# Kernel optimization log

Measured on AMD Instinct MI355X. Metric: run time of the kernel, lower is better.

Reference implementation:

```python
import jax, jax.numpy as jnp
import numpy as np

EPS = 1e-5

def _ln(x, w):
    # LayerNorm over last dim, elementwise affine weight, no bias
    m = jnp.mean(x, axis=-1, keepdims=True)
    v = jnp.mean((x - m) ** 2, axis=-1, keepdims=True)
    return (x - m) * jax.lax.rsqrt(v + EPS) * w

def setup_inputs() -> dict:
    key = jax.random.key(0)
    ks = jax.random.split(key, 16)
    B, NP, NC, E, C = 1, 512, 128, 256, 128
    s = 0.02
    return {
        "z": jax.random.normal(ks[0], (B, NP, NC, E), jnp.float32),
        "protein_pair": jax.random.normal(ks[1], (B, NP, NP, E), jnp.float32),
        "compound_pair": jax.random.normal(ks[2], (B, NC, NC, E), jnp.float32),
        "z_mask": jnp.ones((B, NP, NC, 1), jnp.float32),
        "ln_w": jnp.ones((E,), jnp.float32),
        "lnc_w": jnp.ones((C,), jnp.float32),
        "gw1": jax.random.normal(ks[3], (E, C), jnp.float32) * s,
        "gw2": jax.random.normal(ks[4], (E, C), jnp.float32) * s,
        "w1": jax.random.normal(ks[5], (E, C), jnp.float32) * s,
        "b1": jax.random.normal(ks[6], (C,), jnp.float32) * s,
        "w2": jax.random.normal(ks[7], (E, C), jnp.float32) * s,
        "b2": jax.random.normal(ks[8], (C,), jnp.float32) * s,
        "we": jax.random.normal(ks[9], (E, E), jnp.float32) * s,
        "be": jax.random.normal(ks[10], (E,), jnp.float32) * s,
        "ws": jax.random.normal(ks[11], (C, E), jnp.float32) * s,
        "bs": jax.random.normal(ks[12], (E,), jnp.float32) * s,
    }

def reference(z, protein_pair, compound_pair, z_mask,
              ln_w, lnc_w, gw1, gw2, w1, b1, w2, b2, we, be, ws, bs):
    z = _ln(z, ln_w)                       # [b,Np,Nc,E]
    pp = _ln(protein_pair, ln_w)           # [b,Np,Np,E]
    cp = _ln(compound_pair, ln_w)          # [b,Nc,Nc,E]
    ab1 = jax.nn.sigmoid(z @ gw1) * (z @ w1 + b1) * z_mask   # [b,Np,Nc,c]
    ab2 = jax.nn.sigmoid(z @ gw2) * (z @ w2 + b2) * z_mask   # [b,Np,Nc,c]
    pp = jax.nn.sigmoid(pp @ gw2) * (pp @ w2 + b2)           # [b,Np,Np,c]
    cp = jax.nn.sigmoid(cp @ gw1) * (cp @ w1 + b1)           # [b,Nc,Nc,c]
    g = jax.nn.sigmoid(z @ we + be)                          # [b,Np,Nc,E]
    block1 = jnp.einsum('bikc,bkjc->bijc', pp, ab1)          # [b,Np,Nc,c]
    block2 = jnp.einsum('bikc,bjkc->bijc', ab2, cp)          # [b,Np,Nc,c]
    out = g * (_ln(block1 + block2, lnc_w) @ ws + bs) * z_mask
    return out
```

## Files before the change

### kernel.cpp

```cpp
#include <hip/hip_runtime.h>
#include <hip/hip_bf16.h>

#define NPv 512
#define NCv 128
#define Ev  256
#define Cv  128

typedef __attribute__((ext_vector_type(4))) float f32x4;
typedef __attribute__((ext_vector_type(8))) short s16x8;

__device__ __forceinline__ unsigned short f2bf(float f) {
    union { float f; unsigned u; } v; v.f = f;
    unsigned r = v.u + 0x7fffu + ((v.u >> 16) & 1u);
    return (unsigned short)(r >> 16);
}
__device__ __forceinline__ float bf2f(unsigned short h) {
    union { unsigned u; float f; } v; v.u = ((unsigned)h) << 16;
    return v.f;
}
__device__ __forceinline__ float sigmoidf_(float x) {
    return 1.0f / (1.0f + __expf(-x));
}
__device__ __forceinline__ f32x4 mfma16(s16x8 a, s16x8 b, f32x4 c) {
    return __builtin_amdgcn_mfma_f32_16x16x32_bf16(a, b, c, 0, 0, 0);
}

__global__ void prep_weights(const float* __restrict__ gw1, const float* __restrict__ w1,
                             const float* __restrict__ gw2, const float* __restrict__ w2,
                             const float* __restrict__ we,  const float* __restrict__ wsm,
                             unsigned short* __restrict__ out)
{
    int o = blockIdx.x * 256 + threadIdx.x;
    const float* src; int N, KC; size_t base; int lo;
    if (o < 131072)      { int mi = o >> 15; lo = o & 32767; N = 128; KC = 8;
                           base = (size_t)mi * 32768;
                           src = (mi == 0) ? gw1 : (mi == 1) ? w1 : (mi == 2) ? gw2 : w2; }
    else if (o < 196608) { lo = o - 131072; N = 256; KC = 8; base = 131072; src = we; }
    else                 { lo = o - 196608; N = 256; KC = 4; base = 196608; src = wsm; }
    int e    = lo & 7;
    int lane = (lo >> 3) & 63;
    int blk  = lo >> 9;
    int kc   = blk % KC, nb = blk / KC;
    int n = nb * 16 + (lane & 15);
    int k = kc * 32 + ((lane >> 4) << 3) + e;
    out[base + lo] = f2bf(src[(size_t)k * N + n]);
}

template<int HAS2, int HASG, int HASMASK>
__global__ __launch_bounds__(256, HAS2 ? 3 : 4)
void ln_gate_kernel(const float* __restrict__ X, int M,
                    const float* __restrict__ lnw,
                    const unsigned short* __restrict__ Bu1, const unsigned short* __restrict__ Bv1,
                    const float* __restrict__ bias1, unsigned short* __restrict__ out1,
                    const unsigned short* __restrict__ Bu2, const unsigned short* __restrict__ Bv2,
                    const float* __restrict__ bias2, unsigned short* __restrict__ out2,
                    const unsigned short* __restrict__ Bwe, const float* __restrict__ be,
                    unsigned short* __restrict__ gout,
                    const float* __restrict__ mask)
{
    __shared__ __align__(16) char smem[HAS2 ? (33792 + 18432) : 33792];
    unsigned short (*A_s)[264] = reinterpret_cast<unsigned short(*)[264]>(smem);
    unsigned short (*T_s)[72]  = reinterpret_cast<unsigned short(*)[72]>(
                                     smem + (HAS2 ? 33792 : 0));
    const int t = threadIdx.x;
    const int lane = t & 63, w = t >> 6;
    const int l15 = lane & 15, lg = lane >> 4;
    const int m0 = blockIdx.x * 64;
    const int wy = w >> 1, wx = w & 1;

    float4 lwv[4];
    #pragma unroll
    for (int q = 0; q < 4; q++)
        lwv[q] = *reinterpret_cast<const float4*>(lnw + l15 * 16 + q * 4);
    #pragma unroll
    for (int i = 0; i < 4; i++) {
        const int r = w * 16 + i * 4 + lg;
        const float* xp = X + (size_t)(m0 + r) * Ev + l15 * 16;
        float4 xv[4];
        #pragma unroll
        for (int q = 0; q < 4; q++) xv[q] = *reinterpret_cast<const float4*>(xp + q * 4);
        float s = 0.f, s2 = 0.f;
        #pragma unroll
        for (int q = 0; q < 4; q++) {
            s  += xv[q].x + xv[q].y + xv[q].z + xv[q].w;
            s2 += xv[q].x * xv[q].x + xv[q].y * xv[q].y
                + xv[q].z * xv[q].z + xv[q].w * xv[q].w;
        }
        #pragma unroll
        for (int o = 1; o < 16; o <<= 1) { s += __shfl_xor(s, o); s2 += __shfl_xor(s2, o); }
        float mean = s * (1.0f / Ev);
        float var  = s2 * (1.0f / Ev) - mean * mean;
        float rstd = rsqrtf(var + 1e-5f);
        s16x8 o0, o1;
        #pragma unroll
        for (int q = 0; q < 4; q++) {
            float vx = (xv[q].x - mean) * rstd * lwv[q].x;
            float vy = (xv[q].y - mean) * rstd * lwv[q].y;
            float vz = (xv[q].z - mean) * rstd * lwv[q].z;
            float vw = (xv[q].w - mean) * rstd * lwv[q].w;
            if (q < 2) {
                o0[q * 4 + 0] = (short)f2bf(vx); o0[q * 4 + 1] = (short)f2bf(vy);
                o0[q * 4 + 2] = (short)f2bf(vz); o0[q * 4 + 3] = (short)f2bf(vw);
            } else {
                o1[(q - 2) * 4 + 0] = (short)f2bf(vx); o1[(q - 2) * 4 + 1] = (short)f2bf(vy);
                o1[(q - 2) * 4 + 2] = (short)f2bf(vz); o1[(q - 2) * 4 + 3] = (short)f2bf(vw);
            }
        }
        *reinterpret_cast<s16x8*>(&A_s[r][l15 * 16])     = o0;
        *reinterpret_cast<s16x8*>(&A_s[r][l15 * 16 + 8]) = o1;
    }
    __syncthreads();

    auto gated = [&](const unsigned short* Bu, const unsigned short* Bv,
                     const float* bias, unsigned short* outT) {
        f32x4 au[2][4] = {};
        f32x4 av[2][4] = {};
        for (int kk = 0; kk < Ev; kk += 32) {
            const int kc8 = kk >> 5;
            s16x8 a[2], bu[4], bv[4];
            #pragma unroll
            for (int fi = 0; fi < 2; fi++)
                a[fi] = *reinterpret_cast<const s16x8*>(&A_s[wy * 32 + fi * 16 + l15][kk + lg * 8]);
            #pragma unroll
            for (int fj = 0; fj < 4; fj++) {
                size_t fo = (((size_t)(wx * 4 + fj) * 8 + kc8) * 64 + lane) * 8;
                bu[fj] = *reinterpret_cast<const s16x8*>(Bu + fo);
                bv[fj] = *reinterpret_cast<const s16x8*>(Bv + fo);
            }
            #pragma unroll
            for (int fi = 0; fi < 2; fi++)
                #pragma unroll
                for (int fj = 0; fj < 4; fj++) {
                    au[fi][fj] = mfma16(a[fi], bu[fj], au[fi][fj]);
                    av[fi][fj] = mfma16(a[fi], bv[fj], av[fi][fj]);
                }
        }
        __syncthreads();
        #pragma unroll
        for (int fi = 0; fi < 2; fi++)
            #pragma unroll
            for (int r = 0; r < 4; r++) {
                int ml = wy * 32 + fi * 16 + lg * 4 + r;
                float mval = HASMASK ? mask[m0 + ml] : 1.0f;
                #pragma unroll
                for (int fj = 0; fj < 4; fj++) {
                    int c = wx * 64 + fj * 16 + l15;
                    float val = sigmoidf_(au[fi][fj][r]) * (av[fi][fj][r] + bias[c]);
                    T_s[c][ml] = f2bf(val * mval);
                }
            }
        __syncthreads();
        #pragma unroll
        for (int it = 0; it < 4; it++) {
            int cid = it * 256 + t; int c = cid >> 3, ch = cid & 7;
            *reinterpret_cast<float4*>(outT + (size_t)c * M + m0 + ch * 8) =
                *reinterpret_cast<const float4*>(&T_s[c][ch * 8]);
        }
        __syncthreads();
    };

    gated(Bu1, Bv1, bias1, out1);
    if (HAS2) gated(Bu2, Bv2, bias2, out2);

    if (HASG) {
        unsigned short (*T2g)[144] = reinterpret_cast<unsigned short(*)[144]>(
                                         smem + (HAS2 ? 33792 : 0));
        #pragma unroll
        for (int half = 0; half < 2; half++) {
            f32x4 au[2][4] = {};
            for (int kk = 0; kk < Ev; kk += 32) {
                const int kc8 = kk >> 5;
                s16x8 a[2], bu[4];
                #pragma unroll
                for (int fi = 0; fi < 2; fi++)
                    a[fi] = *reinterpret_cast<const s16x8*>(&A_s[wy * 32 + fi * 16 + l15][kk + lg * 8]);
                #pragma unroll
                for (int fj = 0; fj < 4; fj++) {
                    size_t fo = (((size_t)(half * 8 + wx * 4 + fj) * 8 + kc8) * 64 + lane) * 8;
                    bu[fj] = *reinterpret_cast<const s16x8*>(Bwe + fo);
                }
                #pragma unroll
                for (int fi = 0; fi < 2; fi++)
                    #pragma unroll
                    for (int fj = 0; fj < 4; fj++)
                        au[fi][fj] = mfma16(a[fi], bu[fj], au[fi][fj]);
            }
            __syncthreads();
            #pragma unroll
            for (int fi = 0; fi < 2; fi++)
                #pragma unroll
                for (int fj = 0; fj < 4; fj++) {
                    int np = wx * 64 + fj * 16 + l15;
                    float bev = be[half * 128 + np];
                    #pragma unroll
                    for (int r = 0; r < 4; r++) {
                        int ml = wy * 32 + fi * 16 + lg * 4 + r;
                        T2g[ml][np] = f2bf(sigmoidf_(au[fi][fj][r] + bev));
                    }
                }
            __syncthreads();
            #pragma unroll
            for (int it = 0; it < 4; it++) {
                int cid = it * 256 + t; int m = cid >> 4, ch = cid & 15;
                *reinterpret_cast<float4*>(gout + (size_t)(m0 + m) * Ev + half * 128 + ch * 8) =
                    *reinterpret_cast<const float4*>(&T2g[m][ch * 8]);
            }
            __syncthreads();
        }
    }
}

__global__ void transpose_ab1(const unsigned short* __restrict__ in,
                              unsigned short* __restrict__ out)
{
    __shared__ unsigned short T[64][72];
    const int t = threadIdx.x;
    const int c   = blockIdx.z;
    const int ip0 = blockIdx.x * 64;
    const int jc0 = blockIdx.y * 64;
    const unsigned short* src = in  + (size_t)c * (NPv * NCv);
    unsigned short*       dst = out + (size_t)c * (NPv * NCv);
    #pragma unroll
    for (int it = 0; it < 2; it++) {
        int cid = it * 256 + t; int r = cid >> 3, ch = cid & 7;
        *reinterpret_cast<float4*>(&T[r][ch * 8]) =
            *reinterpret_cast<const float4*>(src + (size_t)(ip0 + r) * NCv + jc0 + ch * 8);
    }
    __syncthreads();
    #pragma unroll
    for (int it = 0; it < 2; it++) {
        int cid = it * 256 + t; int jr = cid >> 3, ch = cid & 7;
        unsigned short v[8];
        #pragma unroll
        for (int e = 0; e < 8; e++) v[e] = T[ch * 8 + e][jr];
        *reinterpret_cast<float4*>(dst + (size_t)(jc0 + jr) * NPv + ip0 + ch * 8) =
            *reinterpret_cast<const float4*>(v);
    }
}

__global__ __launch_bounds__(256, 2)
void block_kernel(const unsigned short* __restrict__ ppt,
                  const unsigned short* __restrict__ ab1tt,
                  const unsigned short* __restrict__ ab2t,
                  const unsigned short* __restrict__ cpt,
                  float* __restrict__ blockT)
{
    __shared__ unsigned short A_s[128][40];
    __shared__ unsigned short B_s[128][40];
    const int t = threadIdx.x, lane = t & 63, w = t >> 6;
    const int l15 = lane & 15, lg = lane >> 4;
    const int i0 = blockIdx.x * 128;
    const int c  = blockIdx.y;
    const int wy = w >> 1, wx = w & 1;
    f32x4 acc[4][4] = {};

    const unsigned short* pa = ppt   + (size_t)c * (NPv * NPv);
    const unsigned short* pb = ab1tt + (size_t)c * (NCv * NPv);
    for (int kk = 0; kk < NPv; kk += 32) {
        __syncthreads();
        #pragma unroll
        for (int it = 0; it < 2; it++) {
            int cid = it * 256 + t; int r = cid >> 2, ch = cid & 3;
            *reinterpret_cast<float4*>(&A_s[r][ch * 8]) =
                *reinterpret_cast<const float4*>(pa + (size_t)(i0 + r) * NPv + kk + ch * 8);
            *reinterpret_cast<float4*>(&B_s[r][ch * 8]) =
                *reinterpret_cast<const float4*>(pb + (size_t)r * NPv + kk + ch * 8);
        }
        __syncthreads();
        s16x8 a[4], b[4];
        #pragma unroll
        for (int f = 0; f < 4; f++) {
            a[f] = *reinterpret_cast<const s16x8*>(&A_s[wy * 64 + f * 16 + l15][lg * 8]);
            b[f] = *reinterpret_cast<const s16x8*>(&B_s[wx * 64 + f * 16 + l15][lg * 8]);
        }
        #pragma unroll
        for (int fi = 0; fi < 4; fi++)
            #pragma unroll
            for (int fj = 0; fj < 4; fj++)
                acc[fi][fj] = mfma16(a[fi], b[fj], acc[fi][fj]);
    }

    const unsigned short* pa2 = ab2t + (size_t)c * (NPv * NCv);
    const unsigned short* pb2 = cpt  + (size_t)c * (NCv * NCv);
    for (int kk = 0; kk < NCv; kk += 32) {
        __syncthreads();
        #pragma unroll
        for (int it = 0; it < 2; it++) {
            int cid = it * 256 + t; int r = cid >> 2, ch = cid & 3;
            *reinterpret_cast<float4*>(&A_s[r][ch * 8]) =
                *reinterpret_cast<const float4*>(pa2 + (size_t)(i0 + r) * NCv + kk + ch * 8);
            *reinterpret_cast<float4*>(&B_s[r][ch * 8]) =
                *reinterpret_cast<const float4*>(pb2 + (size_t)r * NCv + kk + ch * 8);
        }
        __syncthreads();
        s16x8 a[4], b[4];
        #pragma unroll
        for (int f = 0; f < 4; f++) {
            a[f] = *reinterpret_cast<const s16x8*>(&A_s[wy * 64 + f * 16 + l15][lg * 8]);
            b[f] = *reinterpret_cast<const s16x8*>(&B_s[wx * 64 + f * 16 + l15][lg * 8]);
        }
        #pragma unroll
        for (int fi = 0; fi < 4; fi++)
            #pragma unroll
            for (int fj = 0; fj < 4; fj++)
                acc[fi][fj] = mfma16(a[fi], b[fj], acc[fi][fj]);
    }

    float* dst = blockT + (size_t)c * (NPv * NCv);
    #pragma unroll
    for (int fi = 0; fi < 4; fi++)
        #pragma unroll
        for (int fj = 0; fj < 4; fj++) {
            int jc = wx * 64 + fj * 16 + l15;
            #pragma unroll
            for (int r = 0; r < 4; r++) {
                int il = wy * 64 + fi * 16 + lg * 4 + r;
                dst[(size_t)(i0 + il) * NCv + jc] = acc[fi][fj][r];
            }
        }
}

__global__ __launch_bounds__(256, 2)
void final_kernel(const float* __restrict__ blockT,
                  const unsigned short* __restrict__ gbuf,
                  const unsigned short* __restrict__ wst,
                  const float* __restrict__ lncw,
                  const float* __restrict__ bs,
                  const float* __restrict__ mask,
                  float* __restrict__ out)
{
    __shared__ float Bl[128][68];
    __shared__ unsigned short A_s[64][136];
    __shared__ float red[8][64];
    const int t = threadIdx.x, lane = t & 63, w = t >> 6;
    const int l15 = lane & 15, lg = lane >> 4;
    const int m0 = blockIdx.x * 64;

    #pragma unroll
    for (int it = 0; it < 8; it++) {
        int cid = it * 256 + t; int c = cid >> 4, ch = cid & 15;
        *reinterpret_cast<float4*>(&Bl[c][ch * 4]) =
            *reinterpret_cast<const float4*>(blockT + (size_t)c * 65536 + m0 + ch * 4);
    }
    __syncthreads();

    const int m = t & 63, part = t >> 6;
    float s = 0.f, s2 = 0.f;
    for (int c = part * 32; c < part * 32 + 32; c++) { float v = Bl[c][m]; s += v; s2 += v * v; }
    red[part][m] = s; red[4 + part][m] = s2;
    __syncthreads();
    float ss  = red[0][m] + red[1][m] + red[2][m] + red[3][m];
    float ss2 = red[4][m] + red[5][m] + red[6][m] + red[7][m];
    float mean = ss * (1.0f / 128.0f);
    float var  = ss2 * (1.0f / 128.0f) - mean * mean;
    float rstd = rsqrtf(var + 1e-5f);
    for (int c = part * 32; c < part * 32 + 32; c++)
        A_s[m][c] = f2bf((Bl[c][m] - mean) * rstd * lncw[c]);
    __syncthreads();

    const int wy = w >> 1, wx = w & 1;
    f32x4 acc[2][8] = {};
    for (int kk = 0; kk < 128; kk += 32) {
        const int kc4 = kk >> 5;
        s16x8 a[2], b[8];
        #pragma unroll
        for (int fi = 0; fi < 2; fi++)
            a[fi] = *reinterpret_cast<const s16x8*>(&A_s[wy * 32 + fi * 16 + l15][kk + lg * 8]);
        #pragma unroll
        for (int fj = 0; fj < 8; fj++) {
            size_t fo = (((size_t)(wx * 8 + fj) * 4 + kc4) * 64 + lane) * 8;
            b[fj] = *reinterpret_cast<const s16x8*>(wst + fo);
        }
        #pragma unroll
        for (int fi = 0; fi < 2; fi++)
            #pragma unroll
            for (int fj = 0; fj < 8; fj++)
                acc[fi][fj] = mfma16(a[fi], b[fj], acc[fi][fj]);
    }
    #pragma unroll
    for (int fi = 0; fi < 2; fi++)
        #pragma unroll
        for (int fj = 0; fj < 8; fj++) {
            int n = wx * 128 + fj * 16 + l15;
            float bsn = bs[n];
            #pragma unroll
            for (int r = 0; r < 4; r++) {
                int ml = wy * 32 + fi * 16 + lg * 4 + r;
                float gval = bf2f(gbuf[(size_t)(m0 + ml) * Ev + n]);
                out[(size_t)(m0 + ml) * Ev + n] =
                    gval * (acc[fi][fj][r] + bsn) * mask[m0 + ml];
            }
        }
}

extern "C" void kernel_launch(void* const* d_in, const int* in_sizes, int n_in,
                              void* d_out, int out_size, void* d_ws, size_t ws_size,
                              hipStream_t stream)
{
    const float* z    = (const float*)d_in[0];
    const float* ppin = (const float*)d_in[1];
    const float* cpin = (const float*)d_in[2];
    const float* mask = (const float*)d_in[3];
    const float* lnw  = (const float*)d_in[4];
    const float* lncw = (const float*)d_in[5];
    const float* gw1  = (const float*)d_in[6];
    const float* gw2  = (const float*)d_in[7];
    const float* w1   = (const float*)d_in[8];
    const float* b1   = (const float*)d_in[9];
    const float* w2   = (const float*)d_in[10];
    const float* b2   = (const float*)d_in[11];
    const float* we   = (const float*)d_in[12];
    const float* be   = (const float*)d_in[13];
    const float* wsm  = (const float*)d_in[14];
    const float* bs   = (const float*)d_in[15];
    float* out = (float*)d_out;

    char* p = (char*)d_ws;
    auto alloc = [&](size_t bytes) { char* r = p; p += (bytes + 255) & ~(size_t)255; return r; };
    unsigned short* wts    = (unsigned short*)alloc((size_t)229376 * 2);
    unsigned short* abt1   = (unsigned short*)alloc((size_t)128 * 65536 * 2);
    unsigned short* ab2t   = (unsigned short*)alloc((size_t)128 * 65536 * 2);
    unsigned short* ab1tt  = (unsigned short*)alloc((size_t)128 * 65536 * 2);
    unsigned short* pptb   = (unsigned short*)alloc((size_t)128 * 262144 * 2);
    unsigned short* cptb   = (unsigned short*)alloc((size_t)128 * 16384 * 2);
    unsigned short* gbuf   = (unsigned short*)alloc((size_t)65536 * 256 * 2);
    float*          blockT = (float*)alloc((size_t)128 * 65536 * 4);

    unsigned short* gw1t = wts + 0;
    unsigned short* w1t  = wts + 32768;
    unsigned short* gw2t = wts + 65536;
    unsigned short* w2t  = wts + 98304;
    unsigned short* wet  = wts + 131072;
    unsigned short* wst  = wts + 196608;

    hipLaunchKernelGGL(prep_weights, dim3(896), dim3(256), 0, stream,
                       gw1, w1, gw2, w2, we, wsm, wts);
    hipLaunchKernelGGL((ln_gate_kernel<1, 1, 1>), dim3(1024), dim3(256), 0, stream,
                       z, 65536, lnw, gw1t, w1t, b1, abt1, gw2t, w2t, b2, ab2t,
                       wet, be, gbuf, mask);
    hipLaunchKernelGGL((ln_gate_kernel<0, 0, 0>), dim3(4096), dim3(256), 0, stream,
                       ppin, 262144, lnw, gw2t, w2t, b2, pptb,
                       (const unsigned short*)nullptr, (const unsigned short*)nullptr,
                       (const float*)nullptr, (unsigned short*)nullptr,
                       (const unsigned short*)nullptr, (const float*)nullptr,
                       (unsigned short*)nullptr, (const float*)nullptr);
    hipLaunchKernelGGL((ln_gate_kernel<0, 0, 0>), dim3(256), dim3(256), 0, stream,
                       cpin, 16384, lnw, gw1t, w1t, b1, cptb,
                       (const unsigned short*)nullptr, (const unsigned short*)nullptr,
                       (const float*)nullptr, (unsigned short*)nullptr,
                       (const unsigned short*)nullptr, (const float*)nullptr,
                       (unsigned short*)nullptr, (const float*)nullptr);
    hipLaunchKernelGGL(transpose_ab1, dim3(8, 2, 128), dim3(256), 0, stream, abt1, ab1tt);
    hipLaunchKernelGGL(block_kernel, dim3(4, 128), dim3(256), 0, stream,
                       pptb, ab1tt, ab2t, cptb, blockT);
    hipLaunchKernelGGL(final_kernel, dim3(1024), dim3(256), 0, stream,
                       blockT, gbuf, wst, lncw, bs, mask, out);
}
```

Before: 260.3 us.

## Halve block_kernel row tile and stage output through LDS for coalesced stores

The block_kernel tile shrinks from 128 to 64 rows of i, which doubles the grid to 8x128 workgroups and raises launch_bounds occupancy to 4. Per-wave accumulators drop from 4x4 to 2x4 fragments. The epilogue now writes accumulators into a shared-memory C tile that reuses the A/B buffers, then stores them with coalesced float4 writes instead of scattered scalar stores. In exchange, each B tile (ab1/cp) is reloaded twice as often and each workgroup does less MFMA work per load.

```diff
diff --git a/kernel.cpp b/kernel.cpp
--- a/kernel.cpp
+++ b/kernel.cpp
@@ -238,43 +238,47 @@
     }
 }
 
-__global__ __launch_bounds__(256, 2)
+__global__ __launch_bounds__(256, 4)
 void block_kernel(const unsigned short* __restrict__ ppt,
                   const unsigned short* __restrict__ ab1tt,
                   const unsigned short* __restrict__ ab2t,
                   const unsigned short* __restrict__ cpt,
                   float* __restrict__ blockT)
 {
-    __shared__ unsigned short A_s[128][40];
-    __shared__ unsigned short B_s[128][40];
+    __shared__ __align__(16) char smem[33792];
+    unsigned short (*A_s)[40]  = reinterpret_cast<unsigned short(*)[40]>(smem);
+    unsigned short (*B_s)[40]  = reinterpret_cast<unsigned short(*)[40]>(smem + 5120);
+    float (*C_s)[132]          = reinterpret_cast<float(*)[132]>(smem);
     const int t = threadIdx.x, lane = t & 63, w = t >> 6;
     const int l15 = lane & 15, lg = lane >> 4;
-    const int i0 = blockIdx.x * 128;
+    const int i0 = blockIdx.x * 64;
     const int c  = blockIdx.y;
     const int wy = w >> 1, wx = w & 1;
-    f32x4 acc[4][4] = {};
+    f32x4 acc[2][4] = {};
 
     const unsigned short* pa = ppt   + (size_t)c * (NPv * NPv);
     const unsigned short* pb = ab1tt + (size_t)c * (NCv * NPv);
     for (int kk = 0; kk < NPv; kk += 32) {
         __syncthreads();
+        { int r = t >> 2, ch = t & 3;
+          *reinterpret_cast<float4*>(&A_s[r][ch * 8]) =
+              *reinterpret_cast<const float4*>(pa + (size_t)(i0 + r) * NPv + kk + ch * 8); }
         #pragma unroll
         for (int it = 0; it < 2; it++) {
             int cid = it * 256 + t; int r = cid >> 2, ch = cid & 3;
-            *reinterpret_cast<float4*>(&A_s[r][ch * 8]) =
-                *reinterpret_cast<const float4*>(pa + (size_t)(i0 + r) * NPv + kk + ch * 8);
             *reinterpret_cast<float4*>(&B_s[r][ch * 8]) =
                 *reinterpret_cast<const float4*>(pb + (size_t)r * NPv + kk + ch * 8);
         }
         __syncthreads();
-        s16x8 a[4], b[4];
-        #pragma unroll
-        for (int f = 0; f < 4; f++) {
-            a[f] = *reinterpret_cast<const s16x8*>(&A_s[wy * 64 + f * 16 + l15][lg * 8]);
+        s16x8 a[2], b[4];
+        #pragma unroll
+        for (int f = 0; f < 2; f++)
+            a[f] = *reinterpret_cast<const s16x8*>(&A_s[wy * 32 + f * 16 + l15][lg * 8]);
+        #pragma unroll
+        for (int f = 0; f < 4; f++)
             b[f] = *reinterpret_cast<const s16x8*>(&B_s[wx * 64 + f * 16 + l15][lg * 8]);
-        }
-        #pragma unroll
-        for (int fi = 0; fi < 4; fi++)
+        #pragma unroll
+        for (int fi = 0; fi < 2; fi++)
             #pragma unroll
             for (int fj = 0; fj < 4; fj++)
                 acc[fi][fj] = mfma16(a[fi], b[fj], acc[fi][fj]);
@@ -284,40 +288,50 @@
     const unsigned short* pb2 = cpt  + (size_t)c * (NCv * NCv);
     for (int kk = 0; kk < NCv; kk += 32) {
         __syncthreads();
+        { int r = t >> 2, ch = t & 3;
+          *reinterpret_cast<float4*>(&A_s[r][ch * 8]) =
+              *reinterpret_cast<const float4*>(pa2 + (size_t)(i0 + r) * NCv + kk + ch * 8); }
         #pragma unroll
         for (int it = 0; it < 2; it++) {
             int cid = it * 256 + t; int r = cid >> 2, ch = cid & 3;
-            *reinterpret_cast<float4*>(&A_s[r][ch * 8]) =
-                *reinterpret_cast<const float4*>(pa2 + (size_t)(i0 + r) * NCv + kk + ch * 8);
             *reinterpret_cast<float4*>(&B_s[r][ch * 8]) =
                 *reinterpret_cast<const float4*>(pb2 + (size_t)r * NCv + kk + ch * 8);
         }
         __syncthreads();
-        s16x8 a[4], b[4];
-        #pragma unroll
-        for (int f = 0; f < 4; f++) {
-            a[f] = *reinterpret_cast<const s16x8*>(&A_s[wy * 64 + f * 16 + l15][lg * 8]);
+        s16x8 a[2], b[4];
+        #pragma unroll
+        for (int f = 0; f < 2; f++)
+            a[f] = *reinterpret_cast<const s16x8*>(&A_s[wy * 32 + f * 16 + l15][lg * 8]);
+        #pragma unroll
+        for (int f = 0; f < 4; f++)
             b[f] = *reinterpret_cast<const s16x8*>(&B_s[wx * 64 + f * 16 + l15][lg * 8]);
-        }
-        #pragma unroll
-        for (int fi = 0; fi < 4; fi++)
+        #pragma unroll
+        for (int fi = 0; fi < 2; fi++)
             #pragma unroll
             for (int fj = 0; fj < 4; fj++)
                 acc[fi][fj] = mfma16(a[fi], b[fj], acc[fi][fj]);
     }
 
-    float* dst = blockT + (size_t)c * (NPv * NCv);
-    #pragma unroll
-    for (int fi = 0; fi < 4; fi++)
+    __syncthreads();
+    #pragma unroll
+    for (int fi = 0; fi < 2; fi++)
         #pragma unroll
         for (int fj = 0; fj < 4; fj++) {
             int jc = wx * 64 + fj * 16 + l15;
             #pragma unroll
             for (int r = 0; r < 4; r++) {
-                int il = wy * 64 + fi * 16 + lg * 4 + r;
-                dst[(size_t)(i0 + il) * NCv + jc] = acc[fi][fj][r];
-            }
-        }
+                int il = wy * 32 + fi * 16 + lg * 4 + r;
+                C_s[il][jc] = acc[fi][fj][r];
+            }
+        }
+    __syncthreads();
+    float* dst = blockT + (size_t)c * (NPv * NCv) + (size_t)i0 * NCv;
+    #pragma unroll
+    for (int it = 0; it < 8; it++) {
+        int cid = it * 256 + t; int row = cid >> 5, ch = cid & 31;
+        *reinterpret_cast<float4*>(dst + (size_t)row * NCv + ch * 4) =
+            *reinterpret_cast<const float4*>(&C_s[row][ch * 4]);
+    }
 }
 
 __global__ __launch_bounds__(256, 2)
@@ -451,7 +465,7 @@
                        (const unsigned short*)nullptr, (const float*)nullptr,
                        (unsigned short*)nullptr, (const float*)nullptr);
     hipLaunchKernelGGL(transpose_ab1, dim3(8, 2, 128), dim3(256), 0, stream, abt1, ab1tt);
-    hipLaunchKernelGGL(block_kernel, dim3(4, 128), dim3(256), 0, stream,
+    hipLaunchKernelGGL(block_kernel, dim3(8, 128), dim3(256), 0, stream,
                        pptb, ab1tt, ab2t, cptb, blockT);
     hipLaunchKernelGGL(final_kernel, dim3(1024), dim3(256), 0, stream,
                        blockT, gbuf, wst, lncw, bs, mask, out);
```

New measurement: 271.7 us. +4.4%, slower.
